# Kernel optimization log

Hardware: AMD Instinct MI355X
Metric: run time of the kernel (lower is better)

Reference implementation:

```python
import jax, jax.numpy as jnp
import numpy as np

NUM_HEADS = 12
ROPE_BASE = 10000.0


def _rope_cache(u, v, head_dim):
    # u, v: [n, L] normalized coords; P pairs per axis = head_dim // 4
    P = head_dim // 2 // 2
    freqs = jnp.arange(P) / (P - 1 + 1e-09)
    inv = 1.0 / ROPE_BASE ** freqs
    ang_x = jnp.einsum('nl,f->nlf', u, inv)
    ang_y = jnp.einsum('nl,f->nlf', v, inv)
    return jnp.cos(ang_x), jnp.sin(ang_x), jnp.cos(ang_y), jnp.sin(ang_y)


def _rope_apply(t, cos_x, sin_x, cos_y, sin_y):
    # t: [n, L, H, D]
    n, L, H, D = t.shape
    q = t.reshape(n, L, H, D // 2, 2)
    ppa = (D // 2) // 2  # pairs per axis
    qx, qy = jnp.split(q, [ppa], axis=-2)

    def rotate(qp, c, s):
        c = c[:, :, None, :]
        s = s[:, :, None, :]
        x, y = qp[..., 0], qp[..., 1]
        return jnp.stack([x * c - y * s, x * s + y * c], axis=-1)

    qx = rotate(qx, cos_x, sin_x)
    qy = rotate(qy, cos_y, sin_y)
    return jnp.concatenate([qx, qy], axis=-2).reshape(n, L, H, D)


def setup_inputs() -> dict:
    key = jax.random.key(0)
    ks = jax.random.split(key, 10)
    n, L, d = 16, 1024, 768
    H = NUM_HEADS
    D = d // H
    glorot = jax.nn.initializers.xavier_uniform()
    return {
        'inputs_q': jax.random.normal(ks[0], (n, L, d), jnp.float32),
        'inputs_kv': jax.random.normal(ks[1], (n, L, d), jnp.float32),
        'Wq': glorot(ks[2], (d, H, D), jnp.float32),
        'bq': jnp.zeros((H, D), jnp.float32),
        'Wk': glorot(ks[3], (d, H, D), jnp.float32),
        'bk': jnp.zeros((H, D), jnp.float32),
        'Wv': glorot(ks[4], (d, H, D), jnp.float32),
        'bv': jnp.zeros((H, D), jnp.float32),
        'Wo': glorot(ks[5], (H, D, d), jnp.float32),
        'bo': jnp.zeros((d,), jnp.float32),
    }


def reference(inputs_q, inputs_kv, Wq, bq, Wk, bk, Wv, bv, Wo, bo):
    n, L, d = inputs_q.shape
    H = NUM_HEADS
    D = d // H

    q = jnp.einsum('nld,dhk->nlhk', inputs_q, Wq) + bq
    k = jnp.einsum('nld,dhk->nlhk', inputs_kv, Wk) + bk
    v = jnp.einsum('nld,dhk->nlhk', inputs_kv, Wv) + bv

    # square-grid 2D RoPE coordinates (rope_uv=None fallback)
    h = w = int(np.sqrt(L))
    ys, xs = np.mgrid[:h, :w]
    u = jnp.tile(((xs.reshape(-1) + 0.5) / w).astype(np.float32)[None, :], (n, 1))
    vv = jnp.tile(((ys.reshape(-1) + 0.5) / h).astype(np.float32)[None, :], (n, 1))
    cos_x, sin_x, cos_y, sin_y = _rope_cache(u, vv, D)

    q = _rope_apply(q, cos_x, sin_x, cos_y, sin_y)
    k = _rope_apply(k, cos_x, sin_x, cos_y, sin_y)

    scale = 1.0 / jnp.sqrt(jnp.float32(D))
    attn_logits = jnp.einsum('nqhd,nkhd->nhqk', q, k) * scale
    attn = jax.nn.softmax(attn_logits, axis=-1)
    out = jnp.einsum('nhqk,nkhd->nqhd', attn, v)
    return jnp.einsum('nqhd,hdm->nqm', out, Wo) + bo
```

## Files before the change

kernel.cpp:

```cpp
#include <hip/hip_runtime.h>
#include <cmath>

#define DMODEL 768
#define SEQ    1024
#define NH     12
#define HDIM   64
#define MTOT   16384

typedef unsigned short ushort_t;
typedef __attribute__((ext_vector_type(8))) short short8v;
typedef __attribute__((ext_vector_type(4))) float f32x4;
typedef __attribute__((ext_vector_type(16))) float f32x16;
typedef __attribute__((ext_vector_type(2))) int i32x2v;

union v8u { short8v v; unsigned u[4]; };

__device__ __forceinline__ ushort_t bf16rn(float x) {
  unsigned u = __float_as_uint(x);
  return (ushort_t)((u + 0x7FFFu + ((u >> 16) & 1u)) >> 16);
}
__device__ __forceinline__ void bsplit(float x, ushort_t& h, ushort_t& l) {
  h = bf16rn(x);
  float hf = __uint_as_float((unsigned)h << 16);
  l = bf16rn(x - hf);
}

__device__ __forceinline__ unsigned cvt_pk_bf16(float a, float b) {
  unsigned r;
  asm("v_cvt_pk_bf16_f32 %0, %1, %2" : "=v"(r) : "v"(a), "v"(b));
  return r;
}
__device__ __forceinline__ void bsplit2(float x0, float x1, unsigned& hw, unsigned& lw) {
  hw = cvt_pk_bf16(x0, x1);
  const float h0 = __uint_as_float(hw << 16);
  const float h1 = __uint_as_float(hw & 0xFFFF0000u);
  lw = cvt_pk_bf16(x0 - h0, x1 - h1);
}

__device__ __forceinline__ float vmax3(float a, float b, float c) {
  float d;
  asm("v_max3_f32 %0, %1, %2, %3" : "=v"(d) : "v"(a), "v"(b), "v"(c));
  return d;
}

__device__ __forceinline__ i32x2v pl32(unsigned a, unsigned b) {
  return __builtin_amdgcn_permlane32_swap((int)a, (int)b, false, false);
}

__device__ __forceinline__ void gld16(const void* g, void* l) {
  __builtin_amdgcn_global_load_lds(
      (const __attribute__((address_space(1))) int*)g,
      (__attribute__((address_space(3))) int*)l, 16, 0, 0);
}

__global__ __launch_bounds__(256)
void rope_table_kernel(float* __restrict__ tab) {
  int idx = blockIdx.x * 256 + threadIdx.x;
  if (idx >= SEQ * 16) return;
  int l = idx >> 4, p = idx & 15;
  double u = ((double)(l & 31) + 0.5) / 32.0;
  double v = ((double)(l >> 5) + 0.5) / 32.0;
  double freq = (double)p / (15.0 + 1e-9);
  double inv = pow(10000.0, -freq);
  tab[idx]         = (float)cos(u * inv);
  tab[16384 + idx] = (float)sin(u * inv);
  tab[32768 + idx] = (float)cos(v * inv);
  tab[49152 + idx] = (float)sin(v * inv);
}

__global__ __launch_bounds__(256)
void wsplit_t_kernel(const float* __restrict__ W, ushort_t* __restrict__ TH,
                     ushort_t* __restrict__ TL) {
  __shared__ __align__(16) float T[64][65];
  const int t = threadIdx.x;
  const int kt = blockIdx.x, nt = blockIdx.y;
  const int r = t >> 2, c4 = (t & 3) * 16;
  const float* src = W + (size_t)(kt * 64 + r) * DMODEL + nt * 64 + c4;
#pragma unroll
  for (int i = 0; i < 16; i += 4)
    *(float4*)&T[r][c4 + i] = *(const float4*)&src[i];
  __syncthreads();
  short8v h0, h1, l0, l1;
#pragma unroll
  for (int i = 0; i < 8; ++i) {
    ushort_t hh, ll;
    bsplit(T[c4 + i][r], hh, ll);
    h0[i] = (short)hh; l0[i] = (short)ll;
  }
#pragma unroll
  for (int i = 0; i < 8; ++i) {
    ushort_t hh, ll;
    bsplit(T[c4 + 8 + i][r], hh, ll);
    h1[i] = (short)hh; l1[i] = (short)ll;
  }
  const size_t o = (size_t)(nt * 64 + r) * DMODEL + kt * 64 + c4;
  *(short8v*)&TH[o] = h0; *(short8v*)&TH[o + 8] = h1;
  *(short8v*)&TL[o] = l0; *(short8v*)&TL[o + 8] = l1;
}

template<int AFP32>
__global__ __launch_bounds__(256)
void gemm_mfma_kernel(const float* __restrict__ Af,
                      const ushort_t* __restrict__ Ahi, const ushort_t* __restrict__ Alo,
                      const ushort_t* __restrict__ Bhi, const ushort_t* __restrict__ Blo,
                      const float* __restrict__ bias, float* __restrict__ Cout,
                      ushort_t* __restrict__ Ohi, ushort_t* __restrict__ Olo,
                      const float* __restrict__ rope, int mode, float oscale) {
  __shared__ __align__(16) unsigned char Araw[16384];
  __shared__ __align__(16) ushort_t Bh[128][32];
  __shared__ __align__(16) ushort_t Bl[128][32];
  ushort_t (*Ah)[32] = (ushort_t(*)[32])Araw;
  ushort_t (*Al)[32] = (ushort_t(*)[32])(Araw + 8192);
  float* Afs = (float*)Araw;

  const int t = threadIdx.x, lane = t & 63, w = t >> 6;
  const int l15 = lane & 15, l4 = lane >> 4;
  const int wm = w >> 1, wn = w & 1;
  const int m0 = blockIdx.y * 128, n0 = blockIdx.x * 128;

  const int crow = t >> 2, ccc = (t & 3) * 8;
  const ushort_t* pBh0 = Bhi + (size_t)(n0 + crow) * DMODEL + ccc;
  const ushort_t* pBh1 = pBh0 + (size_t)64 * DMODEL;
  const ushort_t* pBl0 = Blo + (size_t)(n0 + crow) * DMODEL + ccc;
  const ushort_t* pBl1 = pBl0 + (size_t)64 * DMODEL;
  void* dBh0 = &Bh[crow][ccc];      void* dBh1 = &Bh[crow + 64][ccc];
  void* dBl0 = &Bl[crow][ccc];      void* dBl1 = &Bl[crow + 64][ccc];

  const int sr8 = lane >> 3, sc8 = lane & 7, sg = sc8 ^ sr8;
  const ushort_t* pAh0 = nullptr; const ushort_t* pAh1 = nullptr;
  const ushort_t* pAl0 = nullptr; const ushort_t* pAl1 = nullptr;
  void* dAh0 = nullptr; void* dAh1 = nullptr; void* dAl0 = nullptr; void* dAl1 = nullptr;
  if (!AFP32) {
    pAh0 = Ahi + (size_t)(m0 + crow) * DMODEL + ccc;
    pAh1 = pAh0 + (size_t)64 * DMODEL;
    pAl0 = Alo + (size_t)(m0 + crow) * DMODEL + ccc;
    pAl1 = pAl0 + (size_t)64 * DMODEL;
    dAh0 = &Ah[crow][ccc];  dAh1 = &Ah[crow + 64][ccc];
    dAl0 = &Al[crow][ccc];  dAl1 = &Al[crow + 64][ccc];
  }

  f32x4 acc[4][4] = {};

  for (int ks = 0; ks < DMODEL / 32; ++ks) {
    __syncthreads();
    if (AFP32) {
#pragma unroll
      for (int j = 0; j < 4; ++j) {
        const int row = j * 32 + w * 8 + sr8;
        gld16(Af + (size_t)(m0 + row) * DMODEL + ks * 32 + sg * 4,
              &Afs[row * 32 + sc8 * 4]);
      }
    } else {
      gld16(pAh0, dAh0); gld16(pAh1, dAh1);
      gld16(pAl0, dAl0); gld16(pAl1, dAl1);
      pAh0 += 32; pAh1 += 32; pAl0 += 32; pAl1 += 32;
    }
    gld16(pBh0, dBh0); gld16(pBh1, dBh1);
    gld16(pBl0, dBl0); gld16(pBl1, dBl1);
    pBh0 += 32; pBh1 += 32; pBl0 += 32; pBl1 += 32;
    __syncthreads();

    short8v afh[4], afl[4], bfh[4], bfl[4];
#pragma unroll
    for (int f = 0; f < 4; ++f) {
      if (AFP32) {
        const int row = wm * 64 + f * 16 + l15;
        const int rs = l15 & 7;
        const float* ap = Afs + row * 32;
        const f32x4 x0 = *(const f32x4*)(ap + (((2 * l4)     ^ rs) * 4));
        const f32x4 x1 = *(const f32x4*)(ap + (((2 * l4 + 1) ^ rs) * 4));
        v8u hh, ll;
        bsplit2(x0[0], x0[1], hh.u[0], ll.u[0]);
        bsplit2(x0[2], x0[3], hh.u[1], ll.u[1]);
        bsplit2(x1[0], x1[1], hh.u[2], ll.u[2]);
        bsplit2(x1[2], x1[3], hh.u[3], ll.u[3]);
        afh[f] = hh.v; afl[f] = ll.v;
      } else {
        afh[f] = *(const short8v*)&Ah[wm * 64 + f * 16 + l15][l4 * 8];
        afl[f] = *(const short8v*)&Al[wm * 64 + f * 16 + l15][l4 * 8];
      }
      bfh[f] = *(const short8v*)&Bh[wn * 64 + f * 16 + l15][l4 * 8];
      bfl[f] = *(const short8v*)&Bl[wn * 64 + f * 16 + l15][l4 * 8];
    }
#pragma unroll
    for (int mf = 0; mf < 4; ++mf)
#pragma unroll
      for (int nf = 0; nf < 4; ++nf) {
        acc[mf][nf] = __builtin_amdgcn_mfma_f32_16x16x32_bf16(afh[mf], bfh[nf], acc[mf][nf], 0, 0, 0);
        acc[mf][nf] = __builtin_amdgcn_mfma_f32_16x16x32_bf16(afl[mf], bfh[nf], acc[mf][nf], 0, 0, 0);
        acc[mf][nf] = __builtin_amdgcn_mfma_f32_16x16x32_bf16(afh[mf], bfl[nf], acc[mf][nf], 0, 0, 0);
      }
  }

  float bcol[4];
#pragma unroll
  for (int nf = 0; nf < 4; ++nf) bcol[nf] = bias[n0 + wn * 64 + nf * 16 + l15];

  if (mode == 0) {
#pragma unroll
    for (int mf = 0; mf < 4; ++mf)
#pragma unroll
      for (int r = 0; r < 4; ++r) {
        const int m = m0 + wm * 64 + mf * 16 + l4 * 4 + r;
#pragma unroll
        for (int nf = 0; nf < 4; ++nf)
          Cout[(size_t)m * DMODEL + n0 + wn * 64 + nf * 16 + l15] = acc[mf][nf][r] + bcol[nf];
      }
  } else {
    const int h = blockIdx.x * 2 + wn;
#pragma unroll
    for (int mf = 0; mf < 4; ++mf)
#pragma unroll
      for (int r = 0; r < 4; ++r) {
        const int m = m0 + wm * 64 + mf * 16 + l4 * 4 + r;
        const int l = m & (SEQ - 1);
        const int nb = m >> 10;
        const size_t orow = ((size_t)(nb * NH + h) * SEQ + l) * HDIM;
        float vv[4];
#pragma unroll
        for (int nf = 0; nf < 4; ++nf) {
          float v = acc[mf][nf][r] + bcol[nf];
          if (mode == 1) {
            const float vp = __shfl_xor(v, 1, 64);
            const int tb = (nf < 2) ? 0 : 32768;
            const int pi = (nf & 1) * 8 + (l15 >> 1);
            const float c = rope[tb + l * 16 + pi];
            const float s = rope[tb + 16384 + l * 16 + pi];
            v = (l15 & 1) ? (vp * s + v * c) : (v * c - vp * s);
            v *= oscale;
          }
          vv[nf] = v;
        }
        unsigned h01, l01, h23, l23;
        bsplit2(vv[0], vv[1], h01, l01);
        bsplit2(vv[2], vv[3], h23, l23);
        Ohi[orow + 0 * 16 + l15] = (ushort_t)(h01 & 0xFFFFu);
        Ohi[orow + 1 * 16 + l15] = (ushort_t)(h01 >> 16);
        Ohi[orow + 2 * 16 + l15] = (ushort_t)(h23 & 0xFFFFu);
        Ohi[orow + 3 * 16 + l15] = (ushort_t)(h23 >> 16);
        Olo[orow + 0 * 16 + l15] = (ushort_t)(l01 & 0xFFFFu);
        Olo[orow + 1 * 16 + l15] = (ushort_t)(l01 >> 16);
        Olo[orow + 2 * 16 + l15] = (ushort_t)(l23 & 0xFFFFu);
        Olo[orow + 3 * 16 + l15] = (ushort_t)(l23 >> 16);
      }
  }
}

__global__ __launch_bounds__(256)
void vtrans_kernel(const ushort_t* __restrict__ VH, const ushort_t* __restrict__ VL,
                   ushort_t* __restrict__ TH, ushort_t* __restrict__ TL) {
  __shared__ __align__(16) ushort_t Th[64][72];
  __shared__ __align__(16) ushort_t Tl[64][72];
  const int t = threadIdx.x;
  const int lt = blockIdx.x, h = blockIdx.y, n = blockIdx.z;
  const int r = t >> 2, c = (t & 3) * 16;
  const size_t src = ((size_t)(n * NH + h) * SEQ + lt * 64 + r) * HDIM + c;
  *(short8v*)&Th[r][c]     = *(const short8v*)&VH[src];
  *(short8v*)&Th[r][c + 8] = *(const short8v*)&VH[src + 8];
  *(short8v*)&Tl[r][c]     = *(const short8v*)&VL[src];
  *(short8v*)&Tl[r][c + 8] = *(const short8v*)&VL[src + 8];
  __syncthreads();
  short8v h0, h1, l0, l1;
#pragma unroll
  for (int i = 0; i < 8; ++i) { h0[i] = (short)Th[c + i][r];     l0[i] = (short)Tl[c + i][r]; }
#pragma unroll
  for (int i = 0; i < 8; ++i) { h1[i] = (short)Th[c + 8 + i][r]; l1[i] = (short)Tl[c + 8 + i][r]; }
  const size_t dst = ((size_t)(n * NH + h) * HDIM + r) * SEQ + lt * 64 + c;
  *(short8v*)&TH[dst]     = h0; *(short8v*)&TH[dst + 8] = h1;
  *(short8v*)&TL[dst]     = l0; *(short8v*)&TL[dst + 8] = l1;
}

__global__ __launch_bounds__(256)
void attn_mfma_kernel(const ushort_t* __restrict__ qh, const ushort_t* __restrict__ ql,
                      const ushort_t* __restrict__ kh, const ushort_t* __restrict__ kl,
                      const ushort_t* __restrict__ vth, const ushort_t* __restrict__ vtl,
                      ushort_t* __restrict__ abh, ushort_t* __restrict__ abl) {
  __shared__ __align__(16) ushort_t KHs[2][64][64];
  __shared__ __align__(16) ushort_t KLs[2][64][64];
  __shared__ __align__(16) ushort_t VHs[2][64][64];
  __shared__ __align__(16) ushort_t VLs[2][64][64];

  const int t = threadIdx.x;
  const int lane = t & 63, w = t >> 6;
  const int l31 = lane & 31, l1 = lane >> 5;

  const int bid = blockIdx.x;
  const int xcd = bid & 7, rest = bid >> 3;
  const int qt = rest & 7;
  const int hl = (rest >> 3) * 8 + xcd;
  const int h = hl % NH, n = hl / NH;

  const size_t base = (size_t)(n * NH + h) * (SEQ * HDIM);

  short8v qfh[4], qfl[4];
  {
    const size_t qoff = base + (size_t)(qt * 128 + w * 32 + l31) * HDIM + l1 * 8;
#pragma unroll
    for (int ks = 0; ks < 4; ++ks) {
      qfh[ks] = *(const short8v*)&qh[qoff + ks * 16];
      qfl[ks] = *(const short8v*)&ql[qoff + ks * 16];
    }
  }

  const int srow = lane >> 3;
  const int schk = (lane & 7) ^ srow;
  const int sA = 2 * w, sB = 2 * w + 1;
  const size_t kofA = base + (size_t)(sA * 8 + srow) * HDIM + schk * 8;
  const size_t kofB = base + (size_t)(sB * 8 + srow) * HDIM + schk * 8;
  const size_t vofA = base + (size_t)(sA * 8 + srow) * SEQ + schk * 8;
  const size_t vofB = base + (size_t)(sB * 8 + srow) * SEQ + schk * 8;
  const int drA = sA * 8 + srow, drB = sB * 8 + srow, dc = (lane & 7) * 8;

  f32x16 Oa0 = {}, Oa1 = {};
  f32x16 lpv = {};
  float mrun = 0.0f;

#define ATTN_ISSUE(kt_, b_) do {                                            \
    const size_t ko_ = (size_t)(kt_) * (64 * HDIM);                         \
    const size_t vo_ = (size_t)(kt_) * 64;                                  \
    gld16(kh  + kofA + ko_, &KHs[b_][drA][dc]);                             \
    gld16(kh  + kofB + ko_, &KHs[b_][drB][dc]);                             \
    gld16(kl  + kofA + ko_, &KLs[b_][drA][dc]);                             \
    gld16(kl  + kofB + ko_, &KLs[b_][drB][dc]);                             \
    gld16(vth + vofA + vo_, &VHs[b_][drA][dc]);                             \
    gld16(vth + vofB + vo_, &VHs[b_][drB][dc]);                             \
    gld16(vtl + vofA + vo_, &VLs[b_][drA][dc]);                             \
    gld16(vtl + vofB + vo_, &VLs[b_][drB][dc]);                             \
  } while (0)

  ATTN_ISSUE(0, 0);

  for (int kt = 0; kt < 16; ++kt) {
    const int cur = kt & 1;
    __syncthreads();
    if (kt < 15) ATTN_ISSUE(kt + 1, cur ^ 1);

    f32x16 S0 = {}, S1 = {};
    __builtin_amdgcn_s_setprio(1);
#pragma unroll
    for (int ks = 0; ks < 4; ++ks) {
      const int cc = ((2 * ks + l1) ^ (l31 & 7)) * 8;
      const short8v k0h = *(const short8v*)&KHs[cur][l31][cc];
      const short8v k0l = *(const short8v*)&KLs[cur][l31][cc];
      const short8v k1h = *(const short8v*)&KHs[cur][32 + l31][cc];
      const short8v k1l = *(const short8v*)&KLs[cur][32 + l31][cc];
      S0 = __builtin_amdgcn_mfma_f32_32x32x16_bf16(k0h, qfh[ks], S0, 0, 0, 0);
      S1 = __builtin_amdgcn_mfma_f32_32x32x16_bf16(k1h, qfh[ks], S1, 0, 0, 0);
      S0 = __builtin_amdgcn_mfma_f32_32x32x16_bf16(k0l, qfh[ks], S0, 0, 0, 0);
      S1 = __builtin_amdgcn_mfma_f32_32x32x16_bf16(k1l, qfh[ks], S1, 0, 0, 0);
      S0 = __builtin_amdgcn_mfma_f32_32x32x16_bf16(k0h, qfl[ks], S0, 0, 0, 0);
      S1 = __builtin_amdgcn_mfma_f32_32x32x16_bf16(k1h, qfl[ks], S1, 0, 0, 0);
    }
    __builtin_amdgcn_s_setprio(0);

    const float a0 = vmax3(S0[0],  S0[1],  S0[2]);
    const float a1 = vmax3(S0[3],  S0[4],  S0[5]);
    const float a2 = vmax3(S0[6],  S0[7],  S0[8]);
    const float a3 = vmax3(S0[9],  S0[10], S0[11]);
    const float a4 = vmax3(S0[12], S0[13], S0[14]);
    const float b0 = vmax3(S1[0],  S1[1],  S1[2]);
    const float b1 = vmax3(S1[3],  S1[4],  S1[5]);
    const float b2 = vmax3(S1[6],  S1[7],  S1[8]);
    const float b3 = vmax3(S1[9],  S1[10], S1[11]);
    const float b4 = vmax3(S1[12], S1[13], S1[14]);
    const float c0 = vmax3(a0, a1, a2);
    const float c1 = vmax3(a3, a4, S0[15]);
    const float c2 = vmax3(b0, b1, b2);
    const float c3 = vmax3(b3, b4, S1[15]);
    const float mx = fmaxf(vmax3(c0, c1, c2), c3);

    if (__all((mrun == 0.0f) & (mx <= 30.0f))) {
#pragma unroll
      for (int i = 0; i < 16; ++i) {
        S0[i] = __builtin_amdgcn_exp2f(S0[i]);
        S1[i] = __builtin_amdgcn_exp2f(S1[i]);
      }
      lpv += S0 + S1;
    } else {
      const float om = fmaxf(mx, __shfl_xor(mx, 32));
      const float nm = fmaxf(mrun, om);
      const float scl = __builtin_amdgcn_exp2f(mrun - nm);
      mrun = nm;
#pragma unroll
      for (int i = 0; i < 16; ++i) {
        S0[i] = __builtin_amdgcn_exp2f(S0[i] - nm);
        S1[i] = __builtin_amdgcn_exp2f(S1[i] - nm);
      }
      lpv = lpv * scl + (S0 + S1);
      Oa0 = Oa0 * scl;
      Oa1 = Oa1 * scl;
    }

#pragma unroll
    for (int half = 0; half < 2; ++half) {
      unsigned hx[4], hy[4], lx[4], ly[4];
#pragma unroll
      for (int m = 0; m < 4; ++m) {
        float p0, p1, p2, p3;
        if (half == 0) { p0 = S0[4*m]; p1 = S0[4*m+1]; p2 = S0[4*m+2]; p3 = S0[4*m+3]; }
        else           { p0 = S1[4*m]; p1 = S1[4*m+1]; p2 = S1[4*m+2]; p3 = S1[4*m+3]; }
        bsplit2(p0, p1, hx[m], lx[m]);
        bsplit2(p2, p3, hy[m], ly[m]);
      }
      __builtin_amdgcn_s_setprio(1);
#pragma unroll
      for (int kss = 0; kss < 2; ++kss) {
        const i32x2v rhx = pl32(hx[2*kss], hx[2*kss+1]);
        const i32x2v rhy = pl32(hy[2*kss], hy[2*kss+1]);
        const i32x2v rlx = pl32(lx[2*kss], lx[2*kss+1]);
        const i32x2v rly = pl32(ly[2*kss], ly[2*kss+1]);
        v8u bfh, bfl;
        bfh.u[0] = (unsigned)rhx[0]; bfh.u[1] = (unsigned)rhy[0];
        bfh.u[2] = (unsigned)rhx[1]; bfh.u[3] = (unsigned)rhy[1];
        bfl.u[0] = (unsigned)rlx[0]; bfl.u[1] = (unsigned)rly[0];
        bfl.u[2] = (unsigned)rlx[1]; bfl.u[3] = (unsigned)rly[1];
        const int cc = ((4*half + 2*kss + l1) ^ (l31 & 7)) * 8;
        const short8v v0h = *(const short8v*)&VHs[cur][l31][cc];
        const short8v v0l = *(const short8v*)&VLs[cur][l31][cc];
        const short8v v1h = *(const short8v*)&VHs[cur][32 + l31][cc];
        const short8v v1l = *(const short8v*)&VLs[cur][32 + l31][cc];
        Oa0 = __builtin_amdgcn_mfma_f32_32x32x16_bf16(v0h, bfh.v, Oa0, 0, 0, 0);
        Oa1 = __builtin_amdgcn_mfma_f32_32x32x16_bf16(v1h, bfh.v, Oa1, 0, 0, 0);
        Oa0 = __builtin_amdgcn_mfma_f32_32x32x16_bf16(v0l, bfh.v, Oa0, 0, 0, 0);
        Oa1 = __builtin_amdgcn_mfma_f32_32x32x16_bf16(v1l, bfh.v, Oa1, 0, 0, 0);
        Oa0 = __builtin_amdgcn_mfma_f32_32x32x16_bf16(v0h, bfl.v, Oa0, 0, 0, 0);
        Oa1 = __builtin_amdgcn_mfma_f32_32x32x16_bf16(v1h, bfl.v, Oa1, 0, 0, 0);
      }
      __builtin_amdgcn_s_setprio(0);
    }
  }

  float lp = ((((lpv[0]+lpv[1])+(lpv[2]+lpv[3]))+((lpv[4]+lpv[5])+(lpv[6]+lpv[7])))
           + (((lpv[8]+lpv[9])+(lpv[10]+lpv[11]))+((lpv[12]+lpv[13])+(lpv[14]+lpv[15]))));
  lp += __shfl_xor(lp, 32);
  const float inv = 1.0f / lp;
  const size_t orow = ((size_t)n * SEQ + qt * 128 + w * 32 + l31) * DMODEL + h * HDIM;
#pragma unroll
  for (int jd = 0; jd < 2; ++jd) {
#pragma unroll
    for (int g = 0; g < 4; ++g) {
      float o0, o1, o2, o3;
      if (jd == 0) { o0 = Oa0[4*g]; o1 = Oa0[4*g+1]; o2 = Oa0[4*g+2]; o3 = Oa0[4*g+3]; }
      else         { o0 = Oa1[4*g]; o1 = Oa1[4*g+1]; o2 = Oa1[4*g+2]; o3 = Oa1[4*g+3]; }
      o0 *= inv; o1 *= inv; o2 *= inv; o3 *= inv;
      unsigned h01, l01, h23, l23;
      bsplit2(o0, o1, h01, l01);
      bsplit2(o2, o3, h23, l23);
      const int d = 32 * jd + 8 * g + 4 * l1;
      uint2 sh; sh.x = h01; sh.y = h23;
      uint2 sl; sl.x = l01; sl.y = l23;
      *(uint2*)&abh[orow + d] = sh;
      *(uint2*)&abl[orow + d] = sl;
    }
  }
#undef ATTN_ISSUE
}

extern "C" void kernel_launch(void* const* d_in, const int* in_sizes, int n_in,
                              void* d_out, int out_size, void* d_ws, size_t ws_size,
                              hipStream_t stream) {
  (void)in_sizes; (void)n_in; (void)out_size;
  const float* Xq  = (const float*)d_in[0];
  const float* Xkv = (const float*)d_in[1];
  const float* Wq  = (const float*)d_in[2];
  const float* bq  = (const float*)d_in[3];
  const float* Wk  = (const float*)d_in[4];
  const float* bk  = (const float*)d_in[5];
  const float* Wv  = (const float*)d_in[6];
  const float* bv  = (const float*)d_in[7];
  const float* Wo  = (const float*)d_in[8];
  const float* bo  = (const float*)d_in[9];
  float* out = (float*)d_out;

  if (ws_size < 201588736ull) return;
  char* W = (char*)d_ws;
  const size_t HB = 25165824ull;
  float*    rope = (float*)W;
  ushort_t* vth = (ushort_t*)(W + 262144);
  ushort_t* vtl = (ushort_t*)(W + 262144 + HB);
  char* C0 = W + 262144 + 2 * HB;
  ushort_t* qhi = (ushort_t*)(C0);
  ushort_t* qlo = (ushort_t*)(C0 + HB);
  ushort_t* khi = (ushort_t*)(C0 + 2 * HB);
  ushort_t* klo = (ushort_t*)(C0 + 3 * HB);
  ushort_t* woth = (ushort_t*)(C0);
  ushort_t* wotl = woth + 589824;
  char* D0 = C0 + 4 * HB;
  ushort_t* vbh = (ushort_t*)(D0);
  ushort_t* vbl = (ushort_t*)(D0 + HB);
  ushort_t* abh = vbh;
  ushort_t* abl = vbl;
  ushort_t* wqth = (ushort_t*)d_out;            ushort_t* wqtl = wqth + 589824;
  ushort_t* wkth = wqth + 1179648;              ushort_t* wktl = wkth + 589824;
  ushort_t* wvth = wqth + 2359296;              ushort_t* wvtl = wvth + 589824;

  rope_table_kernel<<<64, 256, 0, stream>>>(rope);
  wsplit_t_kernel<<<dim3(12, 12), 256, 0, stream>>>(Wq, wqth, wqtl);
  wsplit_t_kernel<<<dim3(12, 12), 256, 0, stream>>>(Wk, wkth, wktl);
  wsplit_t_kernel<<<dim3(12, 12), 256, 0, stream>>>(Wv, wvth, wvtl);

  const dim3 gg(DMODEL / 128, MTOT / 128);
  const float q_scale = 0.125f * 1.44269504088896340736f;

  gemm_mfma_kernel<1><<<gg, 256, 0, stream>>>(Xq, nullptr, nullptr, wqth, wqtl,
                                              bq, nullptr, qhi, qlo, rope, 1, q_scale);
  gemm_mfma_kernel<1><<<gg, 256, 0, stream>>>(Xkv, nullptr, nullptr, wkth, wktl,
                                              bk, nullptr, khi, klo, rope, 1, 1.0f);
  gemm_mfma_kernel<1><<<gg, 256, 0, stream>>>(Xkv, nullptr, nullptr, wvth, wvtl,
                                              bv, nullptr, vbh, vbl, rope, 2, 1.0f);

  vtrans_kernel<<<dim3(16, NH, 16), 256, 0, stream>>>(vbh, vbl, vth, vtl);

  attn_mfma_kernel<<<1536, 256, 0, stream>>>(qhi, qlo, khi, klo, vth, vtl, abh, abl);

  wsplit_t_kernel<<<dim3(12, 12), 256, 0, stream>>>(Wo, woth, wotl);
  gemm_mfma_kernel<0><<<gg, 256, 0, stream>>>(nullptr, abh, abl, woth, wotl,
                                              bo, out, nullptr, nullptr, rope, 0, 1.0f);
}
```

Baseline: 569.0 us.

## Fuse V transpose into V projection epilogue and merge prep kernels

```diff
diff --git a/kernel.cpp b/kernel.cpp
--- a/kernel.cpp
+++ b/kernel.cpp
@@ -53,27 +53,10 @@
       (__attribute__((address_space(3))) int*)l, 16, 0, 0);
 }
 
-__global__ __launch_bounds__(256)
-void rope_table_kernel(float* __restrict__ tab) {
-  int idx = blockIdx.x * 256 + threadIdx.x;
-  if (idx >= SEQ * 16) return;
-  int l = idx >> 4, p = idx & 15;
-  double u = ((double)(l & 31) + 0.5) / 32.0;
-  double v = ((double)(l >> 5) + 0.5) / 32.0;
-  double freq = (double)p / (15.0 + 1e-9);
-  double inv = pow(10000.0, -freq);
-  tab[idx]         = (float)cos(u * inv);
-  tab[16384 + idx] = (float)sin(u * inv);
-  tab[32768 + idx] = (float)cos(v * inv);
-  tab[49152 + idx] = (float)sin(v * inv);
-}
-
-__global__ __launch_bounds__(256)
-void wsplit_t_kernel(const float* __restrict__ W, ushort_t* __restrict__ TH,
-                     ushort_t* __restrict__ TL) {
-  __shared__ __align__(16) float T[64][65];
-  const int t = threadIdx.x;
-  const int kt = blockIdx.x, nt = blockIdx.y;
+__device__ __forceinline__
+void wsplit_body(const float* __restrict__ W, ushort_t* __restrict__ TH,
+                 ushort_t* __restrict__ TL, int kt, int nt, int t, float* Tls) {
+  float (*T)[65] = (float(*)[65])Tls;
   const int r = t >> 2, c4 = (t & 3) * 16;
   const float* src = W + (size_t)(kt * 64 + r) * DMODEL + nt * 64 + c4;
 #pragma unroll
@@ -98,7 +81,41 @@
   *(short8v*)&TL[o] = l0; *(short8v*)&TL[o + 8] = l1;
 }
 
-template<int AFP32>
+__global__ __launch_bounds__(256)
+void prep_kernel(float* __restrict__ tab,
+                 const float* __restrict__ Wq, ushort_t* __restrict__ QH, ushort_t* __restrict__ QL,
+                 const float* __restrict__ Wk, ushort_t* __restrict__ KH, ushort_t* __restrict__ KL,
+                 const float* __restrict__ Wv, ushort_t* __restrict__ VH, ushort_t* __restrict__ VL) {
+  __shared__ __align__(16) float Tls[64 * 65];
+  const int bx = blockIdx.x, t = threadIdx.x;
+  if (bx < 64) {
+    int idx = bx * 256 + t;
+    int l = idx >> 4, p = idx & 15;
+    double u = ((double)(l & 31) + 0.5) / 32.0;
+    double v = ((double)(l >> 5) + 0.5) / 32.0;
+    double freq = (double)p / (15.0 + 1e-9);
+    double inv = pow(10000.0, -freq);
+    tab[idx]         = (float)cos(u * inv);
+    tab[16384 + idx] = (float)sin(u * inv);
+    tab[32768 + idx] = (float)cos(v * inv);
+    tab[49152 + idx] = (float)sin(v * inv);
+    return;
+  }
+  const int wi = (bx - 64) / 144, b = (bx - 64) % 144;
+  const int kt = b % 12, nt = b / 12;
+  if (wi == 0)      wsplit_body(Wq, QH, QL, kt, nt, t, Tls);
+  else if (wi == 1) wsplit_body(Wk, KH, KL, kt, nt, t, Tls);
+  else              wsplit_body(Wv, VH, VL, kt, nt, t, Tls);
+}
+
+__global__ __launch_bounds__(256)
+void wsplit_t_kernel(const float* __restrict__ W, ushort_t* __restrict__ TH,
+                     ushort_t* __restrict__ TL) {
+  __shared__ __align__(16) float Tls[64 * 65];
+  wsplit_body(W, TH, TL, blockIdx.x, blockIdx.y, threadIdx.x, Tls);
+}
+
+template<int AFP32, int VT>
 __global__ __launch_bounds__(256)
 void gemm_mfma_kernel(const float* __restrict__ Af,
                       const ushort_t* __restrict__ Ahi, const ushort_t* __restrict__ Alo,
@@ -196,7 +213,57 @@
 #pragma unroll
   for (int nf = 0; nf < 4; ++nf) bcol[nf] = bias[n0 + wn * 64 + nf * 16 + l15];
 
-  if (mode == 0) {
+  if (VT) {
+    ushort_t* hiT = (ushort_t*)Araw;
+    ushort_t* loTa = (ushort_t*)Bh;
+    ushort_t* loTb = (ushort_t*)Bl;
+    const int nb = blockIdx.y >> 3;
+    const int l0 = (blockIdx.y & 7) * 128;
+#pragma unroll
+    for (int hs = 0; hs < 2; ++hs) {
+      __syncthreads();
+      if (wn == hs) {
+#pragma unroll
+        for (int mf = 0; mf < 4; ++mf)
+#pragma unroll
+          for (int r = 0; r < 4; ++r) {
+            const int ll = wm * 64 + mf * 16 + l4 * 4 + r;
+            const int lg = ll >> 3, li = ll & 7;
+            unsigned h01, lo01, h23, lo23;
+            bsplit2(acc[mf][0][r] + bcol[0], acc[mf][1][r] + bcol[1], h01, lo01);
+            bsplit2(acc[mf][2][r] + bcol[2], acc[mf][3][r] + bcol[3], h23, lo23);
+            const ushort_t hv[4] = {(ushort_t)(h01 & 0xFFFFu), (ushort_t)(h01 >> 16),
+                                    (ushort_t)(h23 & 0xFFFFu), (ushort_t)(h23 >> 16)};
+            const ushort_t lv[4] = {(ushort_t)(lo01 & 0xFFFFu), (ushort_t)(lo01 >> 16),
+                                    (ushort_t)(lo23 & 0xFFFFu), (ushort_t)(lo23 >> 16)};
+#pragma unroll
+            for (int nf = 0; nf < 4; ++nf) {
+              const int d = nf * 16 + l15;
+              const int off = ((lg ^ (d & 7)) << 3) + li;
+              hiT[d * 128 + off] = hv[nf];
+              if (nf < 2) loTa[d * 128 + off] = lv[nf];
+              else        loTb[(d - 32) * 128 + off] = lv[nf];
+            }
+          }
+      }
+      __syncthreads();
+      {
+        const int d = t >> 2;
+        const int hglob = blockIdx.x * 2 + hs;
+        const size_t dst = ((size_t)(nb * NH + hglob) * HDIM + d) * SEQ + l0;
+#pragma unroll
+        for (int j = 0; j < 4; ++j) {
+          const int lg = (t & 3) * 4 + j;
+          const int off = (lg ^ (d & 7)) << 3;
+          const short8v hv = *(const short8v*)&hiT[d * 128 + off];
+          const short8v lv = (d < 32) ? *(const short8v*)&loTa[d * 128 + off]
+                                      : *(const short8v*)&loTb[(d - 32) * 128 + off];
+          *(short8v*)&Ohi[dst + lg * 8] = hv;
+          *(short8v*)&Olo[dst + lg * 8] = lv;
+        }
+      }
+    }
+  } else if (mode == 0) {
 #pragma unroll
     for (int mf = 0; mf < 4; ++mf)
 #pragma unroll
@@ -247,30 +314,6 @@
 }
 
 __global__ __launch_bounds__(256)
-void vtrans_kernel(const ushort_t* __restrict__ VH, const ushort_t* __restrict__ VL,
-                   ushort_t* __restrict__ TH, ushort_t* __restrict__ TL) {
-  __shared__ __align__(16) ushort_t Th[64][72];
-  __shared__ __align__(16) ushort_t Tl[64][72];
-  const int t = threadIdx.x;
-  const int lt = blockIdx.x, h = blockIdx.y, n = blockIdx.z;
-  const int r = t >> 2, c = (t & 3) * 16;
-  const size_t src = ((size_t)(n * NH + h) * SEQ + lt * 64 + r) * HDIM + c;
-  *(short8v*)&Th[r][c]     = *(const short8v*)&VH[src];
-  *(short8v*)&Th[r][c + 8] = *(const short8v*)&VH[src + 8];
-  *(short8v*)&Tl[r][c]     = *(const short8v*)&VL[src];
-  *(short8v*)&Tl[r][c + 8] = *(const short8v*)&VL[src + 8];
-  __syncthreads();
-  short8v h0, h1, l0, l1;
-#pragma unroll
-  for (int i = 0; i < 8; ++i) { h0[i] = (short)Th[c + i][r];     l0[i] = (short)Tl[c + i][r]; }
-#pragma unroll
-  for (int i = 0; i < 8; ++i) { h1[i] = (short)Th[c + 8 + i][r]; l1[i] = (short)Tl[c + 8 + i][r]; }
-  const size_t dst = ((size_t)(n * NH + h) * HDIM + r) * SEQ + lt * 64 + c;
-  *(short8v*)&TH[dst]     = h0; *(short8v*)&TH[dst + 8] = h1;
-  *(short8v*)&TL[dst]     = l0; *(short8v*)&TL[dst + 8] = l1;
-}
-
-__global__ __launch_bounds__(256)
 void attn_mfma_kernel(const ushort_t* __restrict__ qh, const ushort_t* __restrict__ ql,
                       const ushort_t* __restrict__ kh, const ushort_t* __restrict__ kl,
                       const ushort_t* __restrict__ vth, const ushort_t* __restrict__ vtl,
@@ -486,34 +529,27 @@
   ushort_t* woth = (ushort_t*)(C0);
   ushort_t* wotl = woth + 589824;
   char* D0 = C0 + 4 * HB;
-  ushort_t* vbh = (ushort_t*)(D0);
-  ushort_t* vbl = (ushort_t*)(D0 + HB);
-  ushort_t* abh = vbh;
-  ushort_t* abl = vbl;
+  ushort_t* abh = (ushort_t*)(D0);
+  ushort_t* abl = (ushort_t*)(D0 + HB);
   ushort_t* wqth = (ushort_t*)d_out;            ushort_t* wqtl = wqth + 589824;
   ushort_t* wkth = wqth + 1179648;              ushort_t* wktl = wkth + 589824;
   ushort_t* wvth = wqth + 2359296;              ushort_t* wvtl = wvth + 589824;
 
-  rope_table_kernel<<<64, 256, 0, stream>>>(rope);
-  wsplit_t_kernel<<<dim3(12, 12), 256, 0, stream>>>(Wq, wqth, wqtl);
-  wsplit_t_kernel<<<dim3(12, 12), 256, 0, stream>>>(Wk, wkth, wktl);
-  wsplit_t_kernel<<<dim3(12, 12), 256, 0, stream>>>(Wv, wvth, wvtl);
+  prep_kernel<<<496, 256, 0, stream>>>(rope, Wq, wqth, wqtl, Wk, wkth, wktl, Wv, wvth, wvtl);
 
   const dim3 gg(DMODEL / 128, MTOT / 128);
   const float q_scale = 0.125f * 1.44269504088896340736f;
 
-  gemm_mfma_kernel<1><<<gg, 256, 0, stream>>>(Xq, nullptr, nullptr, wqth, wqtl,
-                                              bq, nullptr, qhi, qlo, rope, 1, q_scale);
-  gemm_mfma_kernel<1><<<gg, 256, 0, stream>>>(Xkv, nullptr, nullptr, wkth, wktl,
-                                              bk, nullptr, khi, klo, rope, 1, 1.0f);
-  gemm_mfma_kernel<1><<<gg, 256, 0, stream>>>(Xkv, nullptr, nullptr, wvth, wvtl,
-                                              bv, nullptr, vbh, vbl, rope, 2, 1.0f);
-
-  vtrans_kernel<<<dim3(16, NH, 16), 256, 0, stream>>>(vbh, vbl, vth, vtl);
+  gemm_mfma_kernel<1,0><<<gg, 256, 0, stream>>>(Xq, nullptr, nullptr, wqth, wqtl,
+                                                bq, nullptr, qhi, qlo, rope, 1, q_scale);
+  gemm_mfma_kernel<1,0><<<gg, 256, 0, stream>>>(Xkv, nullptr, nullptr, wkth, wktl,
+                                                bk, nullptr, khi, klo, rope, 1, 1.0f);
+  gemm_mfma_kernel<1,1><<<gg, 256, 0, stream>>>(Xkv, nullptr, nullptr, wvth, wvtl,
+                                                bv, nullptr, vth, vtl, rope, 2, 1.0f);
 
   attn_mfma_kernel<<<1536, 256, 0, stream>>>(qhi, qlo, khi, klo, vth, vtl, abh, abl);
 
   wsplit_t_kernel<<<dim3(12, 12), 256, 0, stream>>>(Wo, woth, wotl);
-  gemm_mfma_kernel<0><<<gg, 256, 0, stream>>>(nullptr, abh, abl, woth, wotl,
-                                              bo, out, nullptr, nullptr, rope, 0, 1.0f);
-}
+  gemm_mfma_kernel<0,0><<<gg, 256, 0, stream>>>(nullptr, abh, abl, woth, wotl,
+                                                bo, out, nullptr, nullptr, rope, 0, 1.0f);
+}
```

Measured after the change: 531.1 us. 6.7% less time.
